# Kernel optimization log

Hardware: AMD Instinct MI355X
Metric: run time of the kernel (lower is better)

Reference implementation:

```python
import jax, jax.numpy as jnp
import numpy as np

N = 50000
E = 800000
D = 128
H = 128
C = 2
NUM_GRAPHS = 512
EPS = 1e-5


def setup_inputs() -> dict:
    key = jax.random.key(0)
    ks = jax.random.split(key, 12)
    x = jax.random.normal(ks[0], (N, D), dtype=jnp.float32)
    edge_index = jax.random.randint(ks[1], (2, E), 0, N, dtype=jnp.int64)
    batch = jnp.sort(jax.random.randint(ks[2], (N,), 0, NUM_GRAPHS, dtype=jnp.int64))
    s = 1.0 / np.sqrt(D)
    w1l = jax.random.uniform(ks[3], (D, H), jnp.float32, -s, s)
    w1r = jax.random.uniform(ks[4], (D, H), jnp.float32, -s, s)
    b1 = jax.random.uniform(ks[5], (H,), jnp.float32, -s, s)
    sh = 1.0 / np.sqrt(H)
    w2l = jax.random.uniform(ks[6], (H, H), jnp.float32, -sh, sh)
    w2r = jax.random.uniform(ks[7], (H, H), jnp.float32, -sh, sh)
    b2 = jax.random.uniform(ks[8], (H,), jnp.float32, -sh, sh)
    gamma1 = jnp.ones((H,), jnp.float32)
    beta1 = jnp.zeros((H,), jnp.float32)
    gamma2 = jnp.ones((H,), jnp.float32)
    beta2 = jnp.zeros((H,), jnp.float32)
    wlin = jax.random.uniform(ks[9], (H, C), jnp.float32, -sh, sh)
    blin = jax.random.uniform(ks[10], (C,), jnp.float32, -sh, sh)
    return {"x": x, "edge_index": edge_index, "batch": batch,
            "w1l": w1l, "w1r": w1r, "b1": b1, "gamma1": gamma1, "beta1": beta1,
            "w2l": w2l, "w2r": w2r, "b2": b2, "gamma2": gamma2, "beta2": beta2,
            "wlin": wlin, "blin": blin}


def _sage_conv(x, src, dst, wl, wr, b):
    # mean-aggregate source features at target nodes, then linear
    agg = jax.ops.segment_sum(x[src], dst, num_segments=N)          # [N, F]
    cnt = jax.ops.segment_sum(jnp.ones((src.shape[0],), x.dtype), dst, num_segments=N)
    agg = agg / jnp.maximum(cnt, 1.0)[:, None]
    return agg @ wl + b + x @ wr


def _batch_norm(x, gamma, beta):
    mu = jnp.mean(x, axis=0)
    var = jnp.mean(jnp.square(x - mu), axis=0)  # biased, as torch BN training
    return (x - mu) * (gamma / jnp.sqrt(var + EPS)) + beta


def reference(x, edge_index, batch, w1l, w1r, b1, gamma1, beta1,
              w2l, w2r, b2, gamma2, beta2, wlin, blin):
    src, dst = edge_index[0], edge_index[1]
    h = _sage_conv(x, src, dst, w1l, w1r, b1)
    h = jax.nn.relu(_batch_norm(h, gamma1, beta1))
    h = _sage_conv(h, src, dst, w2l, w2r, b2)
    h = jax.nn.relu(_batch_norm(h, gamma2, beta2))
    # global mean pool over graphs
    pooled = jax.ops.segment_sum(h, batch, num_segments=NUM_GRAPHS)
    cnt = jax.ops.segment_sum(jnp.ones((N,), h.dtype), batch, num_segments=NUM_GRAPHS)
    pooled = pooled / jnp.maximum(cnt, 1.0)[:, None]
    return jax.nn.sigmoid(pooled @ wlin + blin)
```

## Files before the change

kernel.cpp:

```cpp
#include <hip/hip_runtime.h>

#define N_NODES 50000
#define N_EDGES 800000
#define NGRAPH 512
#define MAXDEG 64
#define BN_EPS 1e-5f
#define NTILES 3125

typedef __attribute__((ext_vector_type(8))) short s16x8;
typedef __attribute__((ext_vector_type(4))) float f32x4;

__device__ __forceinline__ ushort bf16_rne(float f) {
  uint u = __float_as_uint(f);
  return (ushort)((u + 0x7FFFu + ((u >> 16) & 1u)) >> 16);
}
__device__ __forceinline__ void bf16split(float f, ushort& h, ushort& l) {
  uint u = __float_as_uint(f);
  uint hb = (u + 0x7FFFu + ((u >> 16) & 1u)) & 0xFFFF0000u;
  h = (ushort)(hb >> 16);
  l = bf16_rne(f - __uint_as_float(hb));
}
__device__ __forceinline__ void acc_pk(float* a, uint4 v) {
  a[0] += __uint_as_float(v.x << 16);
  a[1] += __uint_as_float(v.x & 0xFFFF0000u);
  a[2] += __uint_as_float(v.y << 16);
  a[3] += __uint_as_float(v.y & 0xFFFF0000u);
  a[4] += __uint_as_float(v.z << 16);
  a[5] += __uint_as_float(v.z & 0xFFFF0000u);
  a[6] += __uint_as_float(v.w << 16);
  a[7] += __uint_as_float(v.w & 0xFFFF0000u);
}

__global__ __launch_bounds__(256) void fill_kernel(
    const int* __restrict__ ei, int* __restrict__ cursor, ushort* __restrict__ csr)
{
  int e = blockIdx.x * 256 + threadIdx.x;
  if (e < N_EDGES) {
    int dst = ei[N_EDGES + e];
    int slot = atomicAdd(&cursor[dst], 1);
    if (slot < MAXDEG) csr[dst * MAXDEG + slot] = (ushort)ei[e];
  }
}

__global__ __launch_bounds__(256) void wpack_bounds_kernel(
    const float* __restrict__ w1l, const float* __restrict__ w1r,
    const float* __restrict__ w2l, const float* __restrict__ w2r,
    ushort* __restrict__ Wph, ushort* __restrict__ Wpl,
    const int* __restrict__ batch, int* __restrict__ starts)
{
  if (blockIdx.x == 256) {
    for (int g = threadIdx.x; g <= NGRAPH; g += 256) {
      int lo = 0, hi = N_NODES;
      while (lo < hi) {
        int mid = (lo + hi) >> 1;
        if (batch[mid] < g) lo = mid + 1; else hi = mid;
      }
      starts[g] = lo;
    }
    return;
  }
  int idx = blockIdx.x * 256 + threadIdx.x;
  int layer = idx >> 15;
  int e = idx & 32767;
  int j = e & 7, l = (e >> 3) & 63, t = (e >> 9) & 7, s = e >> 12;
  int k = s * 32 + ((l >> 4) << 3) + j;
  int col = t * 16 + (l & 15);
  const float* wl = layer ? w2l : w1l;
  const float* wr = layer ? w2r : w1r;
  float w = (k < 128) ? wl[k * 128 + col] : wr[(k - 128) * 128 + col];
  ushort h, lo;
  bf16split(w, h, lo);
  Wph[idx] = h;
  Wpl[idx] = lo;
}

__global__ __launch_bounds__(256) void splitx_kernel(
    const float* __restrict__ x, ushort* __restrict__ Ahi)
{
  int i = blockIdx.x * 256 + threadIdx.x;
  if (i >= N_NODES * 32) return;
  int n = i >> 5, j = i & 31;
  float4 v = ((const float4*)x)[i];
  ushort4 h;
  h.x = bf16_rne(v.x); h.y = bf16_rne(v.y);
  h.z = bf16_rne(v.z); h.w = bf16_rne(v.w);
  *(ushort4*)(Ahi + (size_t)n * 256 + 128 + j * 4) = h;
}

__global__ __launch_bounds__(256) void gather_kernel(
    ushort* Ahi,
    const ushort* __restrict__ csr, const int* __restrict__ deg)
{
  int gid = blockIdx.x * 256 + threadIdx.x;
  int n = gid >> 4, j = gid & 15;
  if (n >= N_NODES) return;
  int d = min(deg[n], MAXDEG);
  const ushort* lst = csr + n * MAXDEG;
  float a[8] = {0.f, 0.f, 0.f, 0.f, 0.f, 0.f, 0.f, 0.f};
  int i = 0;
  for (; i + 4 <= d; i += 4) {
    int s0 = lst[i], s1 = lst[i + 1], s2 = lst[i + 2], s3 = lst[i + 3];
    uint4 h0 = *(const uint4*)(Ahi + (size_t)s0 * 256 + 128 + j * 8);
    uint4 h1 = *(const uint4*)(Ahi + (size_t)s1 * 256 + 128 + j * 8);
    uint4 h2 = *(const uint4*)(Ahi + (size_t)s2 * 256 + 128 + j * 8);
    uint4 h3 = *(const uint4*)(Ahi + (size_t)s3 * 256 + 128 + j * 8);
    acc_pk(a, h0); acc_pk(a, h1); acc_pk(a, h2); acc_pk(a, h3);
  }
  for (; i < d; ++i) {
    uint4 h = *(const uint4*)(Ahi + (size_t)lst[i] * 256 + 128 + j * 8);
    acc_pk(a, h);
  }
  float inv = 1.0f / fmaxf((float)d, 1.0f);
  ushort hh[8];
  #pragma unroll
  for (int k = 0; k < 8; ++k) {
    a[k] *= inv;
    hh[k] = bf16_rne(a[k]);
  }
  uint4 ho;
  ho.x = (uint)hh[0] | ((uint)hh[1] << 16);
  ho.y = (uint)hh[2] | ((uint)hh[3] << 16);
  ho.z = (uint)hh[4] | ((uint)hh[5] << 16);
  ho.w = (uint)hh[6] | ((uint)hh[7] << 16);
  *(uint4*)(Ahi + (size_t)n * 256 + j * 8) = ho;
}

__global__ __launch_bounds__(512) void gemm_kernel(
    const ushort* __restrict__ Ahi,
    const ushort* __restrict__ Wph, const ushort* __restrict__ Wpl,
    const float* __restrict__ bias,
    ushort* __restrict__ zb, float* __restrict__ stats)
{
  __shared__ uint4 lds_w[8192];
  __shared__ float lds_stats[256];
  int tid = threadIdx.x;

  {
    const uint4* gh = (const uint4*)Wph;
    const uint4* gl = (const uint4*)Wpl;
    #pragma unroll
    for (int i = 0; i < 8; ++i) lds_w[tid + i * 512] = gh[tid + i * 512];
    #pragma unroll
    for (int i = 0; i < 8; ++i) lds_w[4096 + tid + i * 512] = gl[tid + i * 512];
  }
  if (tid < 256) lds_stats[tid] = 0.f;
  __syncthreads();

  int wave = tid >> 6, lane = tid & 63;
  int col0 = lane & 15, rg = lane >> 4;
  int t0 = blockIdx.x * 16 + wave * 2;
  bool v0 = t0 < NTILES, v1 = (t0 + 1) < NTILES;
  int r0 = min(t0 * 16 + col0, N_NODES - 1);
  int r1 = min(t0 * 16 + 16 + col0, N_NODES - 1);

  const s16x8* W8h = (const s16x8*)lds_w;
  const s16x8* W8l = W8h + 4096;
  const s16x8* pah0 = (const s16x8*)Ahi + (size_t)r0 * 32 + rg;
  const s16x8* pah1 = (const s16x8*)Ahi + (size_t)r1 * 32 + rg;

  f32x4 acc0[8], acc1[8];
  #pragma unroll
  for (int t = 0; t < 8; ++t) {
    float bc = bias[t * 16 + col0];
    acc0[t] = (f32x4){bc, bc, bc, bc};
    acc1[t] = acc0[t];
  }

  for (int s = 0; s < 8; ++s) {
    s16x8 ah0 = pah0[s * 4];
    s16x8 ah1 = pah1[s * 4];
    #pragma unroll
    for (int t = 0; t < 8; ++t) {
      s16x8 wh = W8h[(s * 8 + t) * 64 + lane];
      s16x8 wo = W8l[(s * 8 + t) * 64 + lane];
      acc0[t] = __builtin_amdgcn_mfma_f32_16x16x32_bf16(ah0, wh, acc0[t], 0, 0, 0);
      acc0[t] = __builtin_amdgcn_mfma_f32_16x16x32_bf16(ah0, wo, acc0[t], 0, 0, 0);
      acc1[t] = __builtin_amdgcn_mfma_f32_16x16x32_bf16(ah1, wh, acc1[t], 0, 0, 0);
      acc1[t] = __builtin_amdgcn_mfma_f32_16x16x32_bf16(ah1, wo, acc1[t], 0, 0, 0);
    }
  }

  float psum[8], psq[8];
  #pragma unroll
  for (int t = 0; t < 8; ++t) { psum[t] = 0.f; psq[t] = 0.f; }
  if (v0) {
    #pragma unroll
    for (int t = 0; t < 8; ++t) {
      #pragma unroll
      for (int r = 0; r < 4; ++r) {
        float v = acc0[t][r];
        zb[(size_t)(t0 * 16 + rg * 4 + r) * 128 + t * 16 + col0] = bf16_rne(v);
        psum[t] += v; psq[t] += v * v;
      }
    }
  }
  if (v1) {
    #pragma unroll
    for (int t = 0; t < 8; ++t) {
      #pragma unroll
      for (int r = 0; r < 4; ++r) {
        float v = acc1[t][r];
        zb[(size_t)(t0 * 16 + 16 + rg * 4 + r) * 128 + t * 16 + col0] = bf16_rne(v);
        psum[t] += v; psq[t] += v * v;
      }
    }
  }

  #pragma unroll
  for (int t = 0; t < 8; ++t) {
    atomicAdd(&lds_stats[t * 16 + col0], psum[t]);
    atomicAdd(&lds_stats[128 + t * 16 + col0], psq[t]);
  }
  __syncthreads();
  if (tid < 256) atomicAdd(&stats[tid], lds_stats[tid]);
}

__global__ __launch_bounds__(128) void finalize_kernel(
    const float* __restrict__ stats, const float* __restrict__ gamma,
    const float* __restrict__ beta, float* __restrict__ scsh)
{
  int f = threadIdx.x;
  const float invN = 1.0f / (float)N_NODES;
  float mu = stats[f] * invN;
  float var = stats[128 + f] * invN - mu * mu;
  var = fmaxf(var, 0.f);
  float s = gamma[f] * rsqrtf(var + BN_EPS);
  scsh[f] = s;
  scsh[128 + f] = beta[f] - mu * s;
}

__global__ __launch_bounds__(256) void bnrelu_split_kernel(
    const ushort* __restrict__ zb, const float* __restrict__ scsh,
    ushort* __restrict__ Ahi)
{
  int i = blockIdx.x * 256 + threadIdx.x;
  if (i >= N_NODES * 16) return;
  int n = i >> 4, g8 = i & 15;
  uint4 v = *(const uint4*)(zb + (size_t)n * 128 + g8 * 8);
  float4 sA = *(const float4*)(scsh + g8 * 8);
  float4 sB = *(const float4*)(scsh + g8 * 8 + 4);
  float4 tA = *(const float4*)(scsh + 128 + g8 * 8);
  float4 tB = *(const float4*)(scsh + 128 + g8 * 8 + 4);
  float z0 = __uint_as_float(v.x << 16), z1 = __uint_as_float(v.x & 0xFFFF0000u);
  float z2 = __uint_as_float(v.y << 16), z3 = __uint_as_float(v.y & 0xFFFF0000u);
  float z4 = __uint_as_float(v.z << 16), z5 = __uint_as_float(v.z & 0xFFFF0000u);
  float z6 = __uint_as_float(v.w << 16), z7 = __uint_as_float(v.w & 0xFFFF0000u);
  z0 = fmaxf(0.f, fmaf(z0, sA.x, tA.x));
  z1 = fmaxf(0.f, fmaf(z1, sA.y, tA.y));
  z2 = fmaxf(0.f, fmaf(z2, sA.z, tA.z));
  z3 = fmaxf(0.f, fmaf(z3, sA.w, tA.w));
  z4 = fmaxf(0.f, fmaf(z4, sB.x, tB.x));
  z5 = fmaxf(0.f, fmaf(z5, sB.y, tB.y));
  z6 = fmaxf(0.f, fmaf(z6, sB.z, tB.z));
  z7 = fmaxf(0.f, fmaf(z7, sB.w, tB.w));
  uint4 o;
  o.x = (uint)bf16_rne(z0) | ((uint)bf16_rne(z1) << 16);
  o.y = (uint)bf16_rne(z2) | ((uint)bf16_rne(z3) << 16);
  o.z = (uint)bf16_rne(z4) | ((uint)bf16_rne(z5) << 16);
  o.w = (uint)bf16_rne(z6) | ((uint)bf16_rne(z7) << 16);
  *(uint4*)(Ahi + (size_t)n * 256 + 128 + g8 * 8) = o;
}

__global__ __launch_bounds__(256) void pool_head_kernel(
    const ushort* __restrict__ zb, const int* __restrict__ starts,
    const float* __restrict__ scsh,
    const float* __restrict__ wlin, const float* __restrict__ blin,
    float* __restrict__ out)
{
  __shared__ float pl0[256], pl1[256];
  int g = blockIdx.x;
  int tid = threadIdx.x;
  int p = tid & 63;
  int h4 = tid >> 6;
  int start = starts[g], end = starts[g + 1];
  int cnt = end - start;
  float s0 = scsh[2 * p],       s1 = scsh[2 * p + 1];
  float t0 = scsh[128 + 2 * p], t1 = scsh[128 + 2 * p + 1];
  float a0 = 0.f, a1 = 0.f;
  for (int r = start + h4; r < end; r += 4) {
    uint v = *(const uint*)(zb + (size_t)r * 128 + p * 2);
    float z0 = __uint_as_float(v << 16);
    float z1 = __uint_as_float(v & 0xFFFF0000u);
    a0 += fmaxf(0.f, fmaf(z0, s0, t0));
    a1 += fmaxf(0.f, fmaf(z1, s1, t1));
  }
  pl0[tid] = a0;
  pl1[tid] = a1;
  __syncthreads();
  if (tid < 64) {
    float inv = 1.0f / fmaxf((float)cnt, 1.0f);
    float p0 = (pl0[tid] + pl0[tid + 64] + pl0[tid + 128] + pl0[tid + 192]) * inv;
    float p1 = (pl1[tid] + pl1[tid + 64] + pl1[tid + 128] + pl1[tid + 192]) * inv;
    float b0 = fmaf(p0, wlin[(2 * tid) * 2 + 0], p1 * wlin[(2 * tid + 1) * 2 + 0]);
    float b1 = fmaf(p0, wlin[(2 * tid) * 2 + 1], p1 * wlin[(2 * tid + 1) * 2 + 1]);
    for (int off = 32; off > 0; off >>= 1) {
      b0 += __shfl_down(b0, off, 64);
      b1 += __shfl_down(b1, off, 64);
    }
    if (tid == 0) {
      out[g * 2 + 0] = 1.0f / (1.0f + expf(-(b0 + blin[0])));
      out[g * 2 + 1] = 1.0f / (1.0f + expf(-(b1 + blin[1])));
    }
  }
}

extern "C" void kernel_launch(void* const* d_in, const int* in_sizes, int n_in,
                              void* d_out, int out_size, void* d_ws, size_t ws_size,
                              hipStream_t stream) {
  const float* x    = (const float*)d_in[0];
  const int*   ei   = (const int*)d_in[1];
  const int*   batch= (const int*)d_in[2];
  const float* w1l  = (const float*)d_in[3];
  const float* w1r  = (const float*)d_in[4];
  const float* b1   = (const float*)d_in[5];
  const float* g1   = (const float*)d_in[6];
  const float* be1  = (const float*)d_in[7];
  const float* w2l  = (const float*)d_in[8];
  const float* w2r  = (const float*)d_in[9];
  const float* b2   = (const float*)d_in[10];
  const float* g2   = (const float*)d_in[11];
  const float* be2  = (const float*)d_in[12];
  const float* wlin = (const float*)d_in[13];
  const float* blin = (const float*)d_in[14];
  float* out = (float*)d_out;

  char* ws = (char*)d_ws;
  int*    cursor = (int*)(ws + 0);
  float*  stats  = (float*)(ws + 200000);
  float*  scsh   = (float*)(ws + 202048);
  int*    starts = (int*)(ws + 203072);
  ushort* csr    = (ushort*)(ws + 400000);
  ushort* Ahi    = (ushort*)(ws + 6800000);
  ushort* zb     = (ushort*)(ws + 58000000);
  ushort* Wph    = (ushort*)(ws + 83866240);
  ushort* Wpl    = (ushort*)(ws + 83997312);

  const int eblocks = (N_EDGES + 255) / 256;
  const int nblocks = (N_NODES * 32 + 255) / 256;
  const int gblocks = (N_NODES * 16 + 255) / 256;
  const int bblocks = (N_NODES * 16 + 255) / 256;
  const int gemmblocks = (NTILES + 15) / 16;

  hipMemsetAsync(cursor, 0, 202048, stream);
  fill_kernel<<<eblocks, 256, 0, stream>>>(ei, cursor, csr);
  wpack_bounds_kernel<<<257, 256, 0, stream>>>(w1l, w1r, w2l, w2r, Wph, Wpl,
                                               batch, starts);

  splitx_kernel<<<nblocks, 256, 0, stream>>>(x, Ahi);
  gather_kernel<<<gblocks, 256, 0, stream>>>(Ahi, csr, cursor);
  gemm_kernel<<<gemmblocks, 512, 0, stream>>>(Ahi, Wph, Wpl, b1, zb, stats);
  finalize_kernel<<<1, 128, 0, stream>>>(stats, g1, be1, scsh);
  bnrelu_split_kernel<<<bblocks, 256, 0, stream>>>(zb, scsh, Ahi);

  gather_kernel<<<gblocks, 256, 0, stream>>>(Ahi, csr, cursor);
  gemm_kernel<<<gemmblocks, 512, 0, stream>>>(Ahi, Wph + 32768, Wpl + 32768, b2,
                                              zb, stats + 256);
  finalize_kernel<<<1, 128, 0, stream>>>(stats + 256, g2, be2, scsh);

  pool_head_kernel<<<NGRAPH, 256, 0, stream>>>(zb, starts, scsh, wlin, blin, out);
}
```

Measured before the change: 207.2 us.

## Merge prep kernels into one launch, fold BN finalize into consumers, partition edge fill

Fuses the CSR fill, the x-to-bf16 split, the weight packing and the graph-bounds search into a single prep kernel, cutting three launches. The fill now uses 8x as many blocks, each handling only the edges whose destination falls in one of 8 node ranges, to localize atomics and CSR writes. The BN finalize kernels are removed and every block of the bnrelu and pool kernels recomputes the scale and shift into LDS. This removes launch gaps, at the cost of 8x redundant edge-index reads in the fill and redundant per-block stat math.

```diff
diff --git a/kernel.cpp b/kernel.cpp
--- a/kernel.cpp
+++ b/kernel.cpp
@@ -6,6 +6,9 @@
 #define MAXDEG 64
 #define BN_EPS 1e-5f
 #define NTILES 3125
+#define FILLB 25000
+#define SPLITB 6250
+#define NPR 6250
 
 typedef __attribute__((ext_vector_type(8))) short s16x8;
 typedef __attribute__((ext_vector_type(4))) float f32x4;
@@ -31,60 +34,65 @@
   a[7] += __uint_as_float(v.w & 0xFFFF0000u);
 }
 
-__global__ __launch_bounds__(256) void fill_kernel(
-    const int* __restrict__ ei, int* __restrict__ cursor, ushort* __restrict__ csr)
-{
-  int e = blockIdx.x * 256 + threadIdx.x;
-  if (e < N_EDGES) {
-    int dst = ei[N_EDGES + e];
-    int slot = atomicAdd(&cursor[dst], 1);
-    if (slot < MAXDEG) csr[dst * MAXDEG + slot] = (ushort)ei[e];
-  }
-}
-
-__global__ __launch_bounds__(256) void wpack_bounds_kernel(
+__global__ __launch_bounds__(256) void prep_kernel(
+    const int* __restrict__ ei, int* __restrict__ cursor, ushort* __restrict__ csr,
+    const float* __restrict__ x, ushort* __restrict__ Ahi,
     const float* __restrict__ w1l, const float* __restrict__ w1r,
     const float* __restrict__ w2l, const float* __restrict__ w2r,
     ushort* __restrict__ Wph, ushort* __restrict__ Wpl,
     const int* __restrict__ batch, int* __restrict__ starts)
 {
-  if (blockIdx.x == 256) {
-    for (int g = threadIdx.x; g <= NGRAPH; g += 256) {
-      int lo = 0, hi = N_NODES;
-      while (lo < hi) {
-        int mid = (lo + hi) >> 1;
-        if (batch[mid] < g) lo = mid + 1; else hi = mid;
+  int b = blockIdx.x;
+  if (b < FILLB) {
+    int r = b & 7;
+    int e = (b >> 3) * 256 + threadIdx.x;
+    if (e < N_EDGES) {
+      int dst = ei[N_EDGES + e];
+      if (dst / NPR == r) {
+        int slot = atomicAdd(&cursor[dst], 1);
+        if (slot < MAXDEG) csr[dst * MAXDEG + slot] = (ushort)ei[e];
       }
-      starts[g] = lo;
     }
     return;
   }
-  int idx = blockIdx.x * 256 + threadIdx.x;
-  int layer = idx >> 15;
-  int e = idx & 32767;
-  int j = e & 7, l = (e >> 3) & 63, t = (e >> 9) & 7, s = e >> 12;
-  int k = s * 32 + ((l >> 4) << 3) + j;
-  int col = t * 16 + (l & 15);
-  const float* wl = layer ? w2l : w1l;
-  const float* wr = layer ? w2r : w1r;
-  float w = (k < 128) ? wl[k * 128 + col] : wr[(k - 128) * 128 + col];
-  ushort h, lo;
-  bf16split(w, h, lo);
-  Wph[idx] = h;
-  Wpl[idx] = lo;
-}
-
-__global__ __launch_bounds__(256) void splitx_kernel(
-    const float* __restrict__ x, ushort* __restrict__ Ahi)
-{
-  int i = blockIdx.x * 256 + threadIdx.x;
-  if (i >= N_NODES * 32) return;
-  int n = i >> 5, j = i & 31;
-  float4 v = ((const float4*)x)[i];
-  ushort4 h;
-  h.x = bf16_rne(v.x); h.y = bf16_rne(v.y);
-  h.z = bf16_rne(v.z); h.w = bf16_rne(v.w);
-  *(ushort4*)(Ahi + (size_t)n * 256 + 128 + j * 4) = h;
+  b -= FILLB;
+  if (b < SPLITB) {
+    int i = b * 256 + threadIdx.x;
+    if (i < N_NODES * 32) {
+      int n = i >> 5, j = i & 31;
+      float4 v = ((const float4*)x)[i];
+      ushort4 h;
+      h.x = bf16_rne(v.x); h.y = bf16_rne(v.y);
+      h.z = bf16_rne(v.z); h.w = bf16_rne(v.w);
+      *(ushort4*)(Ahi + (size_t)n * 256 + 128 + j * 4) = h;
+    }
+    return;
+  }
+  b -= SPLITB;
+  if (b < 256) {
+    int idx = b * 256 + threadIdx.x;
+    int layer = idx >> 15;
+    int e = idx & 32767;
+    int j = e & 7, l = (e >> 3) & 63, t = (e >> 9) & 7, s = e >> 12;
+    int k = s * 32 + ((l >> 4) << 3) + j;
+    int col = t * 16 + (l & 15);
+    const float* wl = layer ? w2l : w1l;
+    const float* wr = layer ? w2r : w1r;
+    float w = (k < 128) ? wl[k * 128 + col] : wr[(k - 128) * 128 + col];
+    ushort h, lo;
+    bf16split(w, h, lo);
+    Wph[idx] = h;
+    Wpl[idx] = lo;
+    return;
+  }
+  for (int g = threadIdx.x; g <= NGRAPH; g += 256) {
+    int lo = 0, hi = N_NODES;
+    while (lo < hi) {
+      int mid = (lo + hi) >> 1;
+      if (batch[mid] < g) lo = mid + 1; else hi = mid;
+    }
+    starts[g] = lo;
+  }
 }
 
 __global__ __launch_bounds__(256) void gather_kernel(
@@ -215,32 +223,30 @@
   if (tid < 256) atomicAdd(&stats[tid], lds_stats[tid]);
 }
 
-__global__ __launch_bounds__(128) void finalize_kernel(
-    const float* __restrict__ stats, const float* __restrict__ gamma,
-    const float* __restrict__ beta, float* __restrict__ scsh)
-{
-  int f = threadIdx.x;
-  const float invN = 1.0f / (float)N_NODES;
-  float mu = stats[f] * invN;
-  float var = stats[128 + f] * invN - mu * mu;
-  var = fmaxf(var, 0.f);
-  float s = gamma[f] * rsqrtf(var + BN_EPS);
-  scsh[f] = s;
-  scsh[128 + f] = beta[f] - mu * s;
-}
-
 __global__ __launch_bounds__(256) void bnrelu_split_kernel(
-    const ushort* __restrict__ zb, const float* __restrict__ scsh,
+    const ushort* __restrict__ zb, const float* __restrict__ stats,
+    const float* __restrict__ gamma, const float* __restrict__ beta,
     ushort* __restrict__ Ahi)
 {
-  int i = blockIdx.x * 256 + threadIdx.x;
+  __shared__ float sc[256];
+  int tid = threadIdx.x;
+  {
+    int f = tid & 127;
+    const float invN = 1.0f / (float)N_NODES;
+    float mu = stats[f] * invN;
+    float var = fmaxf(stats[128 + f] * invN - mu * mu, 0.f);
+    float s = gamma[f] * rsqrtf(var + BN_EPS);
+    sc[tid] = (tid < 128) ? s : beta[f] - mu * s;
+  }
+  __syncthreads();
+  int i = blockIdx.x * 256 + tid;
   if (i >= N_NODES * 16) return;
   int n = i >> 4, g8 = i & 15;
   uint4 v = *(const uint4*)(zb + (size_t)n * 128 + g8 * 8);
-  float4 sA = *(const float4*)(scsh + g8 * 8);
-  float4 sB = *(const float4*)(scsh + g8 * 8 + 4);
-  float4 tA = *(const float4*)(scsh + 128 + g8 * 8);
-  float4 tB = *(const float4*)(scsh + 128 + g8 * 8 + 4);
+  float4 sA = *(const float4*)(sc + g8 * 8);
+  float4 sB = *(const float4*)(sc + g8 * 8 + 4);
+  float4 tA = *(const float4*)(sc + 128 + g8 * 8);
+  float4 tB = *(const float4*)(sc + 128 + g8 * 8 + 4);
   float z0 = __uint_as_float(v.x << 16), z1 = __uint_as_float(v.x & 0xFFFF0000u);
   float z2 = __uint_as_float(v.y << 16), z3 = __uint_as_float(v.y & 0xFFFF0000u);
   float z4 = __uint_as_float(v.z << 16), z5 = __uint_as_float(v.z & 0xFFFF0000u);
@@ -263,19 +269,30 @@
 
 __global__ __launch_bounds__(256) void pool_head_kernel(
     const ushort* __restrict__ zb, const int* __restrict__ starts,
-    const float* __restrict__ scsh,
+    const float* __restrict__ stats,
+    const float* __restrict__ gamma, const float* __restrict__ beta,
     const float* __restrict__ wlin, const float* __restrict__ blin,
     float* __restrict__ out)
 {
+  __shared__ float sc[256];
   __shared__ float pl0[256], pl1[256];
   int g = blockIdx.x;
   int tid = threadIdx.x;
+  {
+    int f = tid & 127;
+    const float invN = 1.0f / (float)N_NODES;
+    float mu = stats[f] * invN;
+    float var = fmaxf(stats[128 + f] * invN - mu * mu, 0.f);
+    float s = gamma[f] * rsqrtf(var + BN_EPS);
+    sc[tid] = (tid < 128) ? s : beta[f] - mu * s;
+  }
+  __syncthreads();
   int p = tid & 63;
   int h4 = tid >> 6;
   int start = starts[g], end = starts[g + 1];
   int cnt = end - start;
-  float s0 = scsh[2 * p],       s1 = scsh[2 * p + 1];
-  float t0 = scsh[128 + 2 * p], t1 = scsh[128 + 2 * p + 1];
+  float s0 = sc[2 * p],       s1 = sc[2 * p + 1];
+  float t0 = sc[128 + 2 * p], t1 = sc[128 + 2 * p + 1];
   float a0 = 0.f, a1 = 0.f;
   for (int r = start + h4; r < end; r += 4) {
     uint v = *(const uint*)(zb + (size_t)r * 128 + p * 2);
@@ -327,7 +344,6 @@
   char* ws = (char*)d_ws;
   int*    cursor = (int*)(ws + 0);
   float*  stats  = (float*)(ws + 200000);
-  float*  scsh   = (float*)(ws + 202048);
   int*    starts = (int*)(ws + 203072);
   ushort* csr    = (ushort*)(ws + 400000);
   ushort* Ahi    = (ushort*)(ws + 6800000);
@@ -335,27 +351,24 @@
   ushort* Wph    = (ushort*)(ws + 83866240);
   ushort* Wpl    = (ushort*)(ws + 83997312);
 
-  const int eblocks = (N_EDGES + 255) / 256;
-  const int nblocks = (N_NODES * 32 + 255) / 256;
   const int gblocks = (N_NODES * 16 + 255) / 256;
   const int bblocks = (N_NODES * 16 + 255) / 256;
   const int gemmblocks = (NTILES + 15) / 16;
+  const int prepblocks = FILLB + SPLITB + 256 + 1;
 
   hipMemsetAsync(cursor, 0, 202048, stream);
-  fill_kernel<<<eblocks, 256, 0, stream>>>(ei, cursor, csr);
-  wpack_bounds_kernel<<<257, 256, 0, stream>>>(w1l, w1r, w2l, w2r, Wph, Wpl,
-                                               batch, starts);
-
-  splitx_kernel<<<nblocks, 256, 0, stream>>>(x, Ahi);
+  prep_kernel<<<prepblocks, 256, 0, stream>>>(ei, cursor, csr, x, Ahi,
+                                              w1l, w1r, w2l, w2r, Wph, Wpl,
+                                              batch, starts);
+
   gather_kernel<<<gblocks, 256, 0, stream>>>(Ahi, csr, cursor);
   gemm_kernel<<<gemmblocks, 512, 0, stream>>>(Ahi, Wph, Wpl, b1, zb, stats);
-  finalize_kernel<<<1, 128, 0, stream>>>(stats, g1, be1, scsh);
-  bnrelu_split_kernel<<<bblocks, 256, 0, stream>>>(zb, scsh, Ahi);
+  bnrelu_split_kernel<<<bblocks, 256, 0, stream>>>(zb, stats, g1, be1, Ahi);
 
   gather_kernel<<<gblocks, 256, 0, stream>>>(Ahi, csr, cursor);
   gemm_kernel<<<gemmblocks, 512, 0, stream>>>(Ahi, Wph + 32768, Wpl + 32768, b2,
                                               zb, stats + 256);
-  finalize_kernel<<<1, 128, 0, stream>>>(stats + 256, g2, be2, scsh);
-
-  pool_head_kernel<<<NGRAPH, 256, 0, stream>>>(zb, starts, scsh, wlin, blin, out);
-}
+
+  pool_head_kernel<<<NGRAPH, 256, 0, stream>>>(zb, starts, stats + 256, g2, be2,
+                                               wlin, blin, out);
+}
```

New measurement: 188.2 us (median of 2 runs). 9.2% less time.
